# Kernel optimization log

Measured on AMD Instinct MI355X. Metric: run time of the kernel, lower is better.

## Reference

```python
import jax, jax.numpy as jnp
import numpy as np

DIM = 256
HEADS = 8


def _ln(x, g, b, eps=1e-5):
    mu = jnp.mean(x, axis=-1, keepdims=True)
    var = jnp.var(x, axis=-1, keepdims=True)
    return (x - mu) * jax.lax.rsqrt(var + eps) * g + b


def setup_inputs() -> dict:
    key = jax.random.key(0)
    ks = jax.random.split(key, 12)
    d = DIM
    s = lambda fan: 1.0 / np.sqrt(fan)
    return {
        "x": jax.random.normal(ks[0], (1, d, 64, 64), dtype=jnp.float32),
        "ln1_g": jnp.ones((d,), jnp.float32),
        "ln1_b": jnp.zeros((d,), jnp.float32),
        "w_qkv": jax.random.normal(ks[1], (3 * d, d), jnp.float32) * s(d),
        "b_qkv": jnp.zeros((3 * d,), jnp.float32),
        "w_proj": jax.random.normal(ks[2], (d, d), jnp.float32) * s(d),
        "b_proj": jnp.zeros((d,), jnp.float32),
        "ln2_g": jnp.ones((d,), jnp.float32),
        "ln2_b": jnp.zeros((d,), jnp.float32),
        "w_mlp1": jax.random.normal(ks[3], (4 * d, d), jnp.float32) * s(d),
        "b_mlp1": jnp.zeros((4 * d,), jnp.float32),
        "w_mlp2": jax.random.normal(ks[4], (d, 4 * d), jnp.float32) * s(4 * d),
        "b_mlp2": jnp.zeros((d,), jnp.float32),
    }


def reference(x, ln1_g, ln1_b, w_qkv, b_qkv, w_proj, b_proj,
              ln2_g, ln2_b, w_mlp1, b_mlp1, w_mlp2, b_mlp2):
    B, C, H, W = x.shape
    hd = HEADS
    d = C // hd
    scale = d ** (-0.5)
    # work channels-last: [B, H, W, C] -> [B, HW, C]
    xl = jnp.transpose(x, (0, 2, 3, 1)).reshape(B, H * W, C)

    # --- attention branch ---
    xn = _ln(xl, ln1_g, ln1_b)
    qkv = jnp.einsum('bnc,oc->bno', xn, w_qkv) + b_qkv  # [B, N, 3C]
    q, k, v = jnp.split(qkv, 3, axis=-1)
    def heads(t):  # [B,N,C] -> [B,h,N,d]
        return jnp.transpose(t.reshape(B, H * W, hd, d), (0, 2, 1, 3))
    q, k, v = heads(q), heads(k), heads(v)
    attn = jax.nn.softmax(jnp.einsum('bhnd,bhmd->bhnm', q, k) * scale, axis=-1)
    out = jnp.einsum('bhnm,bhmd->bhnd', attn, v)  # [B,h,N,d]
    out = jnp.transpose(out, (0, 2, 1, 3)).reshape(B, H * W, C)
    xl = xl + jnp.einsum('bnc,oc->bno', out, w_proj) + b_proj

    # --- MLP branch ---
    xn = _ln(xl, ln2_g, ln2_b)
    h1 = jax.nn.gelu(jnp.einsum('bnc,oc->bno', xn, w_mlp1) + b_mlp1,
                     approximate=False)
    xl = xl + jnp.einsum('bnf,of->bno', h1, w_mlp2) + b_mlp2

    return jnp.transpose(xl.reshape(B, H, W, C), (0, 3, 1, 2))
```

## Files before the change

### kernel.cpp

```cpp
#include <hip/hip_runtime.h>
#include <hip/hip_bf16.h>

typedef __bf16 bf16_t;
typedef __bf16 bf16x8 __attribute__((ext_vector_type(8)));
typedef __bf16 bf16x4 __attribute__((ext_vector_type(4)));
typedef float  f32x4  __attribute__((ext_vector_type(4)));

#define MFMA(a,b,c) __builtin_amdgcn_mfma_f32_16x16x32_bf16((a),(b),(c),0,0,0)

__device__ __forceinline__ size_t pidx(int n, int k, int K) {
  return (size_t)(n >> 4) * (K << 4) + ((k >> 3) << 7) + ((n & 15) << 3) + (k & 7);
}

__global__ __launch_bounds__(256) void cvt_pack_all(const float* __restrict__ w_qkv,
                                                    const float* __restrict__ w_proj,
                                                    const float* __restrict__ w_mlp1,
                                                    const float* __restrict__ w_mlp2,
                                                    bf16_t* __restrict__ wq, bf16_t* __restrict__ wp,
                                                    bf16_t* __restrict__ w1, bf16_t* __restrict__ w2) {
  int b = blockIdx.x;
  const float* src; bf16_t* dst; int t0, ksh;
  if (b < 96)       { src = w_qkv;  dst = wq; ksh = 5; t0 = b * 256; }
  else if (b < 128) { src = w_proj; dst = wp; ksh = 5; t0 = (b - 96) * 256; }
  else if (b < 256) { src = w_mlp1; dst = w1; ksh = 5; t0 = (b - 128) * 256; }
  else              { src = w_mlp2; dst = w2; ksh = 7; t0 = (b - 256) * 256; }
  int t = t0 + threadIdx.x;
  int n = t >> ksh, kb = t & ((1 << ksh) - 1);
  int K = 8 << ksh;
  const float* p = src + (size_t)n * K + kb * 8;
  float4 a = *(const float4*)p;
  float4 c = *(const float4*)(p + 4);
  bf16x8 o = {(bf16_t)a.x, (bf16_t)a.y, (bf16_t)a.z, (bf16_t)a.w,
              (bf16_t)c.x, (bf16_t)c.y, (bf16_t)c.z, (bf16_t)c.w};
  *(bf16x8*)(dst + (size_t)(n >> 4) * (K << 4) + kb * 128 + ((n & 15) << 3)) = o;
}

__global__ __launch_bounds__(256) void transpose_in(const float* __restrict__ src,
                                                    float* __restrict__ dst) {
  __shared__ float tile[32][33];
  int n0 = blockIdx.x * 32, c0 = blockIdx.y * 32;
  int a = threadIdx.x & 31, b = threadIdx.x >> 5;
#pragma unroll
  for (int i = 0; i < 4; ++i) {
    int c = b + i * 8;
    tile[a][c] = src[(size_t)(c0 + c) * 4096 + n0 + a];
  }
  __syncthreads();
#pragma unroll
  for (int i = 0; i < 4; ++i) {
    int r = b + i * 8;
    dst[(size_t)(n0 + r) * 256 + c0 + a] = tile[r][a];
  }
}

__global__ __launch_bounds__(256) void transpose_out(const float* __restrict__ src,
                                                     float* __restrict__ dst) {
  __shared__ float tile[32][33];
  int n0 = blockIdx.x * 32, c0 = blockIdx.y * 32;
  int a = threadIdx.x & 31, b = threadIdx.x >> 5;
#pragma unroll
  for (int i = 0; i < 4; ++i) {
    int n = b + i * 8;
    tile[a][n] = src[(size_t)(n0 + n) * 256 + c0 + a];
  }
  __syncthreads();
#pragma unroll
  for (int i = 0; i < 4; ++i) {
    int c = b + i * 8;
    dst[(size_t)(c0 + c) * 4096 + n0 + a] = tile[c][a];
  }
}

__global__ __launch_bounds__(256) void ln_rows(const float* __restrict__ in,
                                               const float* __restrict__ g,
                                               const float* __restrict__ bta,
                                               bf16_t* __restrict__ out) {
  int row  = blockIdx.x * 4 + (threadIdx.x >> 6);
  int lane = threadIdx.x & 63;
  float4 v = ((const float4*)(in + (size_t)row * 256))[lane];
  float s  = v.x + v.y + v.z + v.w;
  float sq = v.x * v.x + v.y * v.y + v.z * v.z + v.w * v.w;
#pragma unroll
  for (int off = 32; off; off >>= 1) {
    s  += __shfl_xor(s, off);
    sq += __shfl_xor(sq, off);
  }
  float mu  = s * (1.0f / 256.0f);
  float var = sq * (1.0f / 256.0f) - mu * mu;
  float rs  = rsqrtf(var + 1e-5f);
  float4 gg = ((const float4*)g)[lane];
  float4 bb = ((const float4*)bta)[lane];
  bf16x4 o = {(bf16_t)((v.x - mu) * rs * gg.x + bb.x),
              (bf16_t)((v.y - mu) * rs * gg.y + bb.y),
              (bf16_t)((v.z - mu) * rs * gg.z + bb.z),
              (bf16_t)((v.w - mu) * rs * gg.w + bb.w)};
  int k = lane * 4;
  *(bf16x4*)(out + (size_t)(row >> 4) * 4096 + ((k >> 3) << 7) + ((row & 15) << 3) + (k & 7)) = o;
}

template <int K, int EPI, int RPW>
__global__ __launch_bounds__(256) void gemm_bt(const bf16_t* __restrict__ A,
                                               const bf16_t* __restrict__ W,
                                               const float* __restrict__ bias,
                                               const float* __restrict__ resid,
                                               void* __restrict__ outp, int ldn) {
  constexpr int RB = RPW / 16;
  int w = threadIdx.x >> 6, lane = threadIdx.x & 63;
  int quad = lane >> 4, idx = lane & 15;
  int row0 = blockIdx.x * (4 * RPW) + w * RPW;
  int col0 = blockIdx.y * 64;
  f32x4 acc[RB][4];
#pragma unroll
  for (int rb = 0; rb < RB; ++rb)
#pragma unroll
    for (int nb = 0; nb < 4; ++nb) acc[rb][nb] = (f32x4){0.f, 0.f, 0.f, 0.f};
  const bf16_t* abase = A + (size_t)(row0 >> 4) * (K << 4) + quad * 128 + idx * 8;
  const bf16_t* wbase = W + (size_t)(col0 >> 4) * (K << 4) + quad * 128 + idx * 8;
#pragma unroll 4
  for (int k0 = 0; k0 < K; k0 += 32) {
    bf16x8 a[RB];
#pragma unroll
    for (int rb = 0; rb < RB; ++rb)
      a[rb] = *(const bf16x8*)(abase + (size_t)rb * (K << 4) + k0 * 16);
#pragma unroll
    for (int nb = 0; nb < 4; ++nb) {
      bf16x8 b = *(const bf16x8*)(wbase + (size_t)nb * (K << 4) + k0 * 16);
#pragma unroll
      for (int rb = 0; rb < RB; ++rb) acc[rb][nb] = MFMA(a[rb], b, acc[rb][nb]);
    }
  }
#pragma unroll
  for (int nb = 0; nb < 4; ++nb) {
    int c = col0 + nb * 16 + idx;
    float bv = bias[c];
#pragma unroll
    for (int rb = 0; rb < RB; ++rb)
#pragma unroll
      for (int r = 0; r < 4; ++r) {
        int rr = row0 + rb * 16 + quad * 4 + r;
        float v = acc[rb][nb][r] + bv;
        if constexpr (EPI == 1) {
          v = 0.5f * v * (1.0f + erff(v * 0.70710678118654752f));
          ((bf16_t*)outp)[pidx(rr, c, ldn)] = (bf16_t)v;
        } else if constexpr (EPI == 2) {
          ((float*)outp)[(size_t)rr * ldn + c] = v + resid[(size_t)rr * ldn + c];
        } else {
          bf16_t* qh = (bf16_t*)outp;
          bf16_t* kh = qh + 1048576;
          bf16_t* vp = kh + 1048576;
          if (c < 256) {
            qh[(size_t)(c >> 5) * 131072 + rr * 32 + (c & 31)] = (bf16_t)v;
          } else if (c < 512) {
            kh[(size_t)((c - 256) >> 5) * 131072 + rr * 32 + (c & 31)] = (bf16_t)v;
          } else {
            vp[(size_t)((c - 512) >> 5) * 131072 + (rr >> 5) * 1024 + (c & 31) * 32 + (rr & 31)] = (bf16_t)v;
          }
        }
      }
  }
}

#define SPLIT 4
__global__ __launch_bounds__(256, 4) void attn_split(const bf16_t* __restrict__ qkvh,
                                                     float* __restrict__ o_acc,
                                                     float* __restrict__ l_part) {
  __shared__ bf16_t P[4][32][88];
  int w = threadIdx.x >> 6, lane = threadIdx.x & 63;
  int quad = lane >> 4, idx = lane & 15;
  int qt = blockIdx.x & 31;
  int h  = (blockIdx.x >> 5) & 7;
  int sp = blockIdx.x >> 8;
  int qrow = qt * 128 + w * 32;
  const bf16_t* qh = qkvh + (size_t)h * 131072;
  const bf16_t* kh = qh + 8 * 131072;
  const bf16_t* vp = kh + 8 * 131072;
  const float cs = 0.25503518f;
  bf16x8 qr0 = *(const bf16x8*)(qh + (size_t)(qrow + idx) * 32 + quad * 8);
  bf16x8 qr1 = *(const bf16x8*)(qh + (size_t)(qrow + 16 + idx) * 32 + quad * 8);
  bf16x8 qf0, qf1;
#pragma unroll
  for (int j = 0; j < 8; ++j) {
    qf0[j] = (bf16_t)((float)qr0[j] * cs);
    qf1[j] = (bf16_t)((float)qr1[j] * cs);
  }
  float ls0 = 0.f, ls1 = 0.f;
  f32x4 o00 = {0.f,0.f,0.f,0.f}, o01 = {0.f,0.f,0.f,0.f};
  f32x4 o10 = {0.f,0.f,0.f,0.f}, o11 = {0.f,0.f,0.f,0.f};
  const f32x4 zero = {0.f,0.f,0.f,0.f};
  int kbase = sp * 1024;

  bf16x8 kf[4];
#pragma unroll
  for (int kb = 0; kb < 4; ++kb)
    kf[kb] = *(const bf16x8*)(kh + (size_t)(kbase + kb * 16 + idx) * 32 + quad * 8);

  for (int kt = 0; kt < 16; ++kt) {
    int k0 = kbase + kt * 64;
    int k1 = kbase + ((kt + 1) & 15) * 64;
    const bf16_t* vt = vp + (size_t)(k0 >> 5) * 1024 + quad * 8;
    bf16x8 vv0 = *(const bf16x8*)(vt + idx * 32);
    bf16x8 vv1 = *(const bf16x8*)(vt + (idx + 16) * 32);
    bf16x8 vv2 = *(const bf16x8*)(vt + 1024 + idx * 32);
    bf16x8 vv3 = *(const bf16x8*)(vt + 1024 + (idx + 16) * 32);
    bf16x8 kfn[4];
#pragma unroll
    for (int kb = 0; kb < 4; ++kb)
      kfn[kb] = *(const bf16x8*)(kh + (size_t)(k1 + kb * 16 + idx) * 32 + quad * 8);
#pragma unroll
    for (int kb = 0; kb < 4; ++kb) {
      f32x4 s0 = MFMA(kf[kb], qf0, zero);
      f32x4 s1 = MFMA(kf[kb], qf1, zero);
      float a0 = __builtin_amdgcn_exp2f(s0[0]), a1 = __builtin_amdgcn_exp2f(s0[1]);
      float a2 = __builtin_amdgcn_exp2f(s0[2]), a3 = __builtin_amdgcn_exp2f(s0[3]);
      float b0 = __builtin_amdgcn_exp2f(s1[0]), b1 = __builtin_amdgcn_exp2f(s1[1]);
      float b2 = __builtin_amdgcn_exp2f(s1[2]), b3 = __builtin_amdgcn_exp2f(s1[3]);
      ls0 += (a0 + a1) + (a2 + a3);
      ls1 += (b0 + b1) + (b2 + b3);
      bf16x4 pk0 = {(bf16_t)a0, (bf16_t)a1, (bf16_t)a2, (bf16_t)a3};
      bf16x4 pk1 = {(bf16_t)b0, (bf16_t)b1, (bf16_t)b2, (bf16_t)b3};
      *(bf16x4*)&P[w][idx][kb * 16 + quad * 4] = pk0;
      *(bf16x4*)&P[w][16 + idx][kb * 16 + quad * 4] = pk1;
    }
#pragma unroll
    for (int kc = 0; kc < 2; ++kc) {
      bf16x8 pa0 = *(const bf16x8*)&P[w][idx][kc * 32 + quad * 8];
      bf16x8 pa1 = *(const bf16x8*)&P[w][16 + idx][kc * 32 + quad * 8];
      bf16x8 va = kc ? vv2 : vv0;
      bf16x8 vb = kc ? vv3 : vv1;
      o00 = MFMA(pa0, va, o00);
      o01 = MFMA(pa0, vb, o01);
      o10 = MFMA(pa1, va, o10);
      o11 = MFMA(pa1, vb, o11);
    }
#pragma unroll
    for (int kb = 0; kb < 4; ++kb) kf[kb] = kfn[kb];
  }
  ls0 += __shfl_xor(ls0, 16); ls0 += __shfl_xor(ls0, 32);
  ls1 += __shfl_xor(ls1, 16); ls1 += __shfl_xor(ls1, 32);
  if (quad == 0) {
    l_part[((size_t)sp * 8 + h) * 4096 + qrow + idx]      = ls0;
    l_part[((size_t)sp * 8 + h) * 4096 + qrow + 16 + idx] = ls1;
  }
#pragma unroll
  for (int r = 0; r < 4; ++r) {
    int n0 = qrow + quad * 4 + r;
    atomicAdd(&o_acc[(size_t)n0 * 256 + h * 32 + idx],        o00[r]);
    atomicAdd(&o_acc[(size_t)n0 * 256 + h * 32 + 16 + idx],   o01[r]);
    int n1 = n0 + 16;
    atomicAdd(&o_acc[(size_t)n1 * 256 + h * 32 + idx],        o10[r]);
    atomicAdd(&o_acc[(size_t)n1 * 256 + h * 32 + 16 + idx],   o11[r]);
  }
}

__global__ __launch_bounds__(256) void attn_norm(const float* __restrict__ o_acc,
                                                 const float* __restrict__ l_part,
                                                 bf16_t* __restrict__ attn) {
  int i = (blockIdx.x * 256 + threadIdx.x) * 4;
  int n = i >> 8, cc = i & 255, h = cc >> 5;
  float l = 0.f;
#pragma unroll
  for (int s = 0; s < SPLIT; ++s) l += l_part[((size_t)s * 8 + h) * 4096 + n];
  float inv = 1.0f / l;
  float4 v = *(const float4*)(o_acc + i);
  bf16x4 o = {(bf16_t)(v.x * inv), (bf16_t)(v.y * inv),
              (bf16_t)(v.z * inv), (bf16_t)(v.w * inv)};
  *(bf16x4*)(attn + (size_t)(n >> 4) * 4096 + ((cc >> 3) << 7) + ((n & 15) << 3) + (cc & 7)) = o;
}

extern "C" void kernel_launch(void* const* d_in, const int* in_sizes, int n_in,
                              void* d_out, int out_size, void* d_ws, size_t ws_size,
                              hipStream_t stream) {
  const float* x      = (const float*)d_in[0];
  const float* ln1_g  = (const float*)d_in[1];
  const float* ln1_b  = (const float*)d_in[2];
  const float* w_qkv  = (const float*)d_in[3];
  const float* b_qkv  = (const float*)d_in[4];
  const float* w_proj = (const float*)d_in[5];
  const float* b_proj = (const float*)d_in[6];
  const float* ln2_g  = (const float*)d_in[7];
  const float* ln2_b  = (const float*)d_in[8];
  const float* w_mlp1 = (const float*)d_in[9];
  const float* b_mlp1 = (const float*)d_in[10];
  const float* w_mlp2 = (const float*)d_in[11];
  const float* b_mlp2 = (const float*)d_in[12];

  char* ws = (char*)d_ws;
  float*  xl     = (float*)(ws + 0);
  float*  xl2    = (float*)(ws + (4u  << 20));
  bf16_t* xn     = (bf16_t*)(ws + (8u  << 20));
  bf16_t* qkvh   = (bf16_t*)(ws + (10u << 20));
  bf16_t* attn   = (bf16_t*)(ws + (18u << 20));
  bf16_t* wq     = (bf16_t*)(ws + (20u << 20));
  bf16_t* wp     = wq + 196608;
  bf16_t* w1     = wp + 65536;
  bf16_t* w2     = w1 + 262144;
  float*  l_part = (float*)(ws + (22016u << 10));
  float*  o_acc  = xl2;
  bf16_t* xn2    = xn;
  bf16_t* h1     = qkvh;
  float*  y      = xl;

  hipMemsetAsync(o_acc, 0, 4096 * 256 * sizeof(float), stream);
  cvt_pack_all<<<384, 256, 0, stream>>>(w_qkv, w_proj, w_mlp1, w_mlp2, wq, wp, w1, w2);

  transpose_in<<<dim3(128, 8), 256, 0, stream>>>(x, xl);
  ln_rows<<<1024, 256, 0, stream>>>(xl, ln1_g, ln1_b, xn);

  gemm_bt<256, 3, 32><<<dim3(32, 12), 256, 0, stream>>>(xn, wq, b_qkv, nullptr, qkvh, 768);
  attn_split<<<256 * SPLIT, 256, 0, stream>>>(qkvh, o_acc, l_part);
  attn_norm<<<1024, 256, 0, stream>>>(o_acc, l_part, attn);

  gemm_bt<256, 2, 16><<<dim3(64, 4), 256, 0, stream>>>(attn, wp, b_proj, xl, xl2, 256);
  ln_rows<<<1024, 256, 0, stream>>>(xl2, ln2_g, ln2_b, xn2);

  gemm_bt<256, 1, 32><<<dim3(32, 16), 256, 0, stream>>>(xn2, w1, b_mlp1, nullptr, h1, 1024);
  gemm_bt<1024, 2, 16><<<dim3(64, 4), 256, 0, stream>>>(h1, w2, b_mlp2, xl2, y, 256);

  transpose_out<<<dim3(128, 8), 256, 0, stream>>>(y, (float*)d_out);
}
```

Measured before the change: 184.3 us.

## Fuse input transpose with LN, split-K atomic GEMMs, deeper attention split

Merges the input transpose and first layernorm into one kernel that computes row statistics from a shared-memory tile. The projection and MLP2 GEMMs become split-K with atomicAdd into outputs that earlier kernels pre-initialise with residual plus bias, which removes the separate residual read. Attention split goes from 4 to 8 with higher occupancy, and GEMM row tiles shrink to 16 to launch more blocks. The aim is more parallelism and fewer launches, at the cost of extra atomic traffic and a fused_in kernel with only 128 blocks.

```diff
diff --git a/kernel.cpp b/kernel.cpp
--- a/kernel.cpp
+++ b/kernel.cpp
@@ -35,21 +35,60 @@
   *(bf16x8*)(dst + (size_t)(n >> 4) * (K << 4) + kb * 128 + ((n & 15) << 3)) = o;
 }
 
-__global__ __launch_bounds__(256) void transpose_in(const float* __restrict__ src,
-                                                    float* __restrict__ dst) {
-  __shared__ float tile[32][33];
-  int n0 = blockIdx.x * 32, c0 = blockIdx.y * 32;
-  int a = threadIdx.x & 31, b = threadIdx.x >> 5;
-#pragma unroll
-  for (int i = 0; i < 4; ++i) {
-    int c = b + i * 8;
-    tile[a][c] = src[(size_t)(c0 + c) * 4096 + n0 + a];
+__global__ __launch_bounds__(256) void fused_in(const float* __restrict__ x,
+                                                const float* __restrict__ g,
+                                                const float* __restrict__ bta,
+                                                float* __restrict__ xl,
+                                                bf16_t* __restrict__ xn) {
+  __shared__ float tile[256][33];
+  __shared__ float psum[8][32], psq[8][32], mu_s[32], rs_s[32];
+  int t = threadIdx.x, n0 = blockIdx.x * 32;
+  int lane32 = t & 31, grp = t >> 5;
+#pragma unroll
+  for (int it = 0; it < 32; ++it) {
+    int c = grp + it * 8;
+    tile[c][lane32] = x[(size_t)c * 4096 + n0 + lane32];
   }
   __syncthreads();
-#pragma unroll
-  for (int i = 0; i < 4; ++i) {
-    int r = b + i * 8;
-    dst[(size_t)(n0 + r) * 256 + c0 + a] = tile[r][a];
+  float s = 0.f, sq = 0.f;
+#pragma unroll
+  for (int ci = 0; ci < 32; ++ci) {
+    float v = tile[grp * 32 + ci][lane32];
+    s += v; sq += v * v;
+  }
+  psum[grp][lane32] = s; psq[grp][lane32] = sq;
+  __syncthreads();
+  if (t < 32) {
+    float S = 0.f, Q = 0.f;
+#pragma unroll
+    for (int p = 0; p < 8; ++p) { S += psum[p][t]; Q += psq[p][t]; }
+    float mu = S * (1.0f / 256.0f);
+    float var = Q * (1.0f / 256.0f) - mu * mu;
+    mu_s[t] = mu; rs_s[t] = rsqrtf(var + 1e-5f);
+  }
+  __syncthreads();
+  {
+    float mu = mu_s[lane32], rs = rs_s[lane32];
+    int row = n0 + lane32;
+    bf16_t* op = xn + (size_t)(row >> 4) * 4096 + ((row & 15) << 3);
+#pragma unroll
+    for (int cc8 = 0; cc8 < 4; ++cc8) {
+      int c0 = grp * 32 + cc8 * 8;
+      bf16x8 o;
+#pragma unroll
+      for (int j = 0; j < 8; ++j) {
+        int c = c0 + j;
+        o[j] = (bf16_t)((tile[c][lane32] - mu) * rs * g[c] + bta[c]);
+      }
+      *(bf16x8*)(op + ((c0 >> 3) << 7)) = o;
+    }
+  }
+#pragma unroll
+  for (int it = 0; it < 4; ++it) {
+    int j = grp + it * 8;
+#pragma unroll
+    for (int c0 = 0; c0 < 256; c0 += 32)
+      xl[(size_t)(n0 + j) * 256 + c0 + lane32] = tile[c0 + lane32][j];
   }
 }
 
@@ -71,10 +110,13 @@
   }
 }
 
+template <bool INIT>
 __global__ __launch_bounds__(256) void ln_rows(const float* __restrict__ in,
                                                const float* __restrict__ g,
                                                const float* __restrict__ bta,
-                                               bf16_t* __restrict__ out) {
+                                               bf16_t* __restrict__ out,
+                                               float* __restrict__ yinit,
+                                               const float* __restrict__ b2) {
   int row  = blockIdx.x * 4 + (threadIdx.x >> 6);
   int lane = threadIdx.x & 63;
   float4 v = ((const float4*)(in + (size_t)row * 256))[lane];
@@ -96,19 +138,25 @@
               (bf16_t)((v.w - mu) * rs * gg.w + bb.w)};
   int k = lane * 4;
   *(bf16x4*)(out + (size_t)(row >> 4) * 4096 + ((k >> 3) << 7) + ((row & 15) << 3) + (k & 7)) = o;
-}
-
-template <int K, int EPI, int RPW>
+  if constexpr (INIT) {
+    float4 b2v = ((const float4*)b2)[lane];
+    float4 yv = {v.x + b2v.x, v.y + b2v.y, v.z + b2v.z, v.w + b2v.w};
+    ((float4*)(yinit + (size_t)row * 256))[lane] = yv;
+  }
+}
+
+template <int K, int EPI, int RPW, int KS = 1>
 __global__ __launch_bounds__(256) void gemm_bt(const bf16_t* __restrict__ A,
                                                const bf16_t* __restrict__ W,
                                                const float* __restrict__ bias,
-                                               const float* __restrict__ resid,
                                                void* __restrict__ outp, int ldn) {
   constexpr int RB = RPW / 16;
+  constexpr int KLEN = K / KS;
   int w = threadIdx.x >> 6, lane = threadIdx.x & 63;
   int quad = lane >> 4, idx = lane & 15;
   int row0 = blockIdx.x * (4 * RPW) + w * RPW;
   int col0 = blockIdx.y * 64;
+  int kb0 = KS > 1 ? blockIdx.z * KLEN : 0;
   f32x4 acc[RB][4];
 #pragma unroll
   for (int rb = 0; rb < RB; ++rb)
@@ -117,7 +165,7 @@
   const bf16_t* abase = A + (size_t)(row0 >> 4) * (K << 4) + quad * 128 + idx * 8;
   const bf16_t* wbase = W + (size_t)(col0 >> 4) * (K << 4) + quad * 128 + idx * 8;
 #pragma unroll 4
-  for (int k0 = 0; k0 < K; k0 += 32) {
+  for (int k0 = kb0; k0 < kb0 + KLEN; k0 += 32) {
     bf16x8 a[RB];
 #pragma unroll
     for (int rb = 0; rb < RB; ++rb)
@@ -132,7 +180,7 @@
 #pragma unroll
   for (int nb = 0; nb < 4; ++nb) {
     int c = col0 + nb * 16 + idx;
-    float bv = bias[c];
+    float bv = (EPI == 4) ? 0.f : bias[c];
 #pragma unroll
     for (int rb = 0; rb < RB; ++rb)
 #pragma unroll
@@ -142,8 +190,8 @@
         if constexpr (EPI == 1) {
           v = 0.5f * v * (1.0f + erff(v * 0.70710678118654752f));
           ((bf16_t*)outp)[pidx(rr, c, ldn)] = (bf16_t)v;
-        } else if constexpr (EPI == 2) {
-          ((float*)outp)[(size_t)rr * ldn + c] = v + resid[(size_t)rr * ldn + c];
+        } else if constexpr (EPI == 4) {
+          atomicAdd(&((float*)outp)[(size_t)rr * ldn + c], v);
         } else {
           bf16_t* qh = (bf16_t*)outp;
           bf16_t* kh = qh + 1048576;
@@ -160,11 +208,11 @@
   }
 }
 
-#define SPLIT 4
-__global__ __launch_bounds__(256, 4) void attn_split(const bf16_t* __restrict__ qkvh,
+#define SPLIT 8
+__global__ __launch_bounds__(256, 8) void attn_split(const bf16_t* __restrict__ qkvh,
                                                      float* __restrict__ o_acc,
                                                      float* __restrict__ l_part) {
-  __shared__ bf16_t P[4][32][88];
+  __shared__ bf16_t P[4][32][72];
   int w = threadIdx.x >> 6, lane = threadIdx.x & 63;
   int quad = lane >> 4, idx = lane & 15;
   int qt = blockIdx.x & 31;
@@ -187,16 +235,16 @@
   f32x4 o00 = {0.f,0.f,0.f,0.f}, o01 = {0.f,0.f,0.f,0.f};
   f32x4 o10 = {0.f,0.f,0.f,0.f}, o11 = {0.f,0.f,0.f,0.f};
   const f32x4 zero = {0.f,0.f,0.f,0.f};
-  int kbase = sp * 1024;
+  int kbase = sp * 512;
 
   bf16x8 kf[4];
 #pragma unroll
   for (int kb = 0; kb < 4; ++kb)
     kf[kb] = *(const bf16x8*)(kh + (size_t)(kbase + kb * 16 + idx) * 32 + quad * 8);
 
-  for (int kt = 0; kt < 16; ++kt) {
+  for (int kt = 0; kt < 8; ++kt) {
     int k0 = kbase + kt * 64;
-    int k1 = kbase + ((kt + 1) & 15) * 64;
+    int k1 = kbase + ((kt + 1) & 7) * 64;
     const bf16_t* vt = vp + (size_t)(k0 >> 5) * 1024 + quad * 8;
     bf16x8 vv0 = *(const bf16x8*)(vt + idx * 32);
     bf16x8 vv1 = *(const bf16x8*)(vt + (idx + 16) * 32);
@@ -244,16 +292,18 @@
 #pragma unroll
   for (int r = 0; r < 4; ++r) {
     int n0 = qrow + quad * 4 + r;
-    atomicAdd(&o_acc[(size_t)n0 * 256 + h * 32 + idx],        o00[r]);
-    atomicAdd(&o_acc[(size_t)n0 * 256 + h * 32 + 16 + idx],   o01[r]);
+    atomicAdd(&o_acc[(size_t)n0 * 256 + h * 32 + idx],      o00[r]);
+    atomicAdd(&o_acc[(size_t)n0 * 256 + h * 32 + 16 + idx], o01[r]);
     int n1 = n0 + 16;
-    atomicAdd(&o_acc[(size_t)n1 * 256 + h * 32 + idx],        o10[r]);
-    atomicAdd(&o_acc[(size_t)n1 * 256 + h * 32 + 16 + idx],   o11[r]);
-  }
-}
-
-__global__ __launch_bounds__(256) void attn_norm(const float* __restrict__ o_acc,
+    atomicAdd(&o_acc[(size_t)n1 * 256 + h * 32 + idx],      o10[r]);
+    atomicAdd(&o_acc[(size_t)n1 * 256 + h * 32 + 16 + idx], o11[r]);
+  }
+}
+
+__global__ __launch_bounds__(256) void attn_norm(float* __restrict__ o,
                                                  const float* __restrict__ l_part,
+                                                 const float* __restrict__ xl,
+                                                 const float* __restrict__ bias,
                                                  bf16_t* __restrict__ attn) {
   int i = (blockIdx.x * 256 + threadIdx.x) * 4;
   int n = i >> 8, cc = i & 255, h = cc >> 5;
@@ -261,10 +311,14 @@
 #pragma unroll
   for (int s = 0; s < SPLIT; ++s) l += l_part[((size_t)s * 8 + h) * 4096 + n];
   float inv = 1.0f / l;
-  float4 v = *(const float4*)(o_acc + i);
-  bf16x4 o = {(bf16_t)(v.x * inv), (bf16_t)(v.y * inv),
-              (bf16_t)(v.z * inv), (bf16_t)(v.w * inv)};
-  *(bf16x4*)(attn + (size_t)(n >> 4) * 4096 + ((cc >> 3) << 7) + ((n & 15) << 3) + (cc & 7)) = o;
+  float4 v = *(const float4*)(o + i);
+  bf16x4 ov = {(bf16_t)(v.x * inv), (bf16_t)(v.y * inv),
+               (bf16_t)(v.z * inv), (bf16_t)(v.w * inv)};
+  *(bf16x4*)(attn + (size_t)(n >> 4) * 4096 + ((cc >> 3) << 7) + ((n & 15) << 3) + (cc & 7)) = ov;
+  float4 r = *(const float4*)(xl + i);
+  float4 bb = *(const float4*)(bias + cc);
+  float4 init = {r.x + bb.x, r.y + bb.y, r.z + bb.z, r.w + bb.w};
+  *(float4*)(o + i) = init;
 }
 
 extern "C" void kernel_launch(void* const* d_in, const int* in_sizes, int n_in,
@@ -294,7 +348,7 @@
   bf16_t* wp     = wq + 196608;
   bf16_t* w1     = wp + 65536;
   bf16_t* w2     = w1 + 262144;
-  float*  l_part = (float*)(ws + (22016u << 10));
+  float*  l_part = (float*)(ws + (8u << 20));
   float*  o_acc  = xl2;
   bf16_t* xn2    = xn;
   bf16_t* h1     = qkvh;
@@ -303,18 +357,17 @@
   hipMemsetAsync(o_acc, 0, 4096 * 256 * sizeof(float), stream);
   cvt_pack_all<<<384, 256, 0, stream>>>(w_qkv, w_proj, w_mlp1, w_mlp2, wq, wp, w1, w2);
 
-  transpose_in<<<dim3(128, 8), 256, 0, stream>>>(x, xl);
-  ln_rows<<<1024, 256, 0, stream>>>(xl, ln1_g, ln1_b, xn);
-
-  gemm_bt<256, 3, 32><<<dim3(32, 12), 256, 0, stream>>>(xn, wq, b_qkv, nullptr, qkvh, 768);
+  fused_in<<<128, 256, 0, stream>>>(x, ln1_g, ln1_b, xl, xn);
+
+  gemm_bt<256, 3, 16><<<dim3(64, 12), 256, 0, stream>>>(xn, wq, b_qkv, qkvh, 768);
   attn_split<<<256 * SPLIT, 256, 0, stream>>>(qkvh, o_acc, l_part);
-  attn_norm<<<1024, 256, 0, stream>>>(o_acc, l_part, attn);
-
-  gemm_bt<256, 2, 16><<<dim3(64, 4), 256, 0, stream>>>(attn, wp, b_proj, xl, xl2, 256);
-  ln_rows<<<1024, 256, 0, stream>>>(xl2, ln2_g, ln2_b, xn2);
-
-  gemm_bt<256, 1, 32><<<dim3(32, 16), 256, 0, stream>>>(xn2, w1, b_mlp1, nullptr, h1, 1024);
-  gemm_bt<1024, 2, 16><<<dim3(64, 4), 256, 0, stream>>>(h1, w2, b_mlp2, xl2, y, 256);
+  attn_norm<<<1024, 256, 0, stream>>>(o_acc, l_part, xl, b_proj, attn);
+
+  gemm_bt<256, 4, 16, 2><<<dim3(64, 4, 2), 256, 0, stream>>>(attn, wp, nullptr, xl2, 256);
+  ln_rows<true><<<1024, 256, 0, stream>>>(xl2, ln2_g, ln2_b, xn2, y, b_mlp2);
+
+  gemm_bt<256, 1, 16><<<dim3(64, 16), 256, 0, stream>>>(xn2, w1, b_mlp1, h1, 1024);
+  gemm_bt<1024, 4, 16, 4><<<dim3(64, 4, 4), 256, 0, stream>>>(h1, w2, nullptr, y, 256);
 
   transpose_out<<<dim3(128, 8), 256, 0, stream>>>(y, (float*)d_out);
 }
```

Measured after the change: 313.2 us. 69.9% more time.
